# Performance work log

Hardware: AMD Instinct MI355X
Metric: run time of the kernel (lower is better)

Reference implementation:

```python
import jax, jax.numpy as jnp
import numpy as np

B = 1024          # batch
N = 2048          # number of gene groups
G = 32            # uniform group size (sum of gene_groups = N*G = 65536)
H1 = 2048         # hidden1_size
H2 = 512          # hidden2_size
EPS = 1e-5        # BatchNorm eps
SLOPE = 0.05      # LeakyReLU negative slope


def lrelu(v):
    return jnp.where(v >= 0, v, SLOPE * v)


def setup_inputs() -> dict:
    key = jax.random.key(0)
    ks = jax.random.split(key, 12)
    x = jax.random.normal(ks[0], (B, N * G), dtype=jnp.float32)
    # per-group Linear(G, 1) weights, stacked: [N, G] weights + [N] biases
    Wg = jax.random.normal(ks[1], (N, G), dtype=jnp.float32) / np.sqrt(G)
    bg = jax.random.normal(ks[2], (N,), dtype=jnp.float32) * 0.01
    att_w = jax.random.normal(ks[3], (N,), dtype=jnp.float32)
    W1 = jax.random.normal(ks[4], (N, H1), dtype=jnp.float32) / np.sqrt(N)
    b1 = jnp.zeros((H1,), dtype=jnp.float32)
    W2 = jax.random.normal(ks[5], (H1, H2), dtype=jnp.float32) / np.sqrt(H1)
    b2 = jnp.zeros((H2,), dtype=jnp.float32)
    Wo = jax.random.normal(ks[6], (H2, 1), dtype=jnp.float32) / np.sqrt(H2)
    bo = jnp.zeros((1,), dtype=jnp.float32)
    gamma1 = jnp.ones((H1,), dtype=jnp.float32)
    beta1 = jnp.zeros((H1,), dtype=jnp.float32)
    gamma2 = jnp.ones((H2,), dtype=jnp.float32)
    beta2 = jnp.zeros((H2,), dtype=jnp.float32)
    return dict(x=x, Wg=Wg, bg=bg, att_w=att_w, W1=W1, b1=b1,
                gamma1=gamma1, beta1=beta1, W2=W2, b2=b2,
                gamma2=gamma2, beta2=beta2, Wo=Wo, bo=bo)


def batchnorm(h, gamma, beta):
    # training-mode BatchNorm1d: batch statistics, biased variance
    mu = jnp.mean(h, axis=0)
    var = jnp.mean(jnp.square(h - mu), axis=0)
    return (h - mu) * jax.lax.rsqrt(var + EPS) * gamma + beta


def reference(x, Wg, bg, att_w, W1, b1, gamma1, beta1, W2, b2, gamma2, beta2, Wo, bo):
    # fused per-group linear + LeakyReLU: x viewed as [B, N, G]
    xg = x.reshape(B, N, G)
    g = lrelu(jnp.einsum('bng,ng->bn', xg, Wg) + bg)       # [B, N]
    att = jax.nn.softmax(att_w)                             # [N]
    a = g * att                                             # [B, N]
    h1 = lrelu(batchnorm(a @ W1 + b1, gamma1, beta1))       # [B, H1]
    h2 = lrelu(batchnorm(h1 @ W2 + b2, gamma2, beta2))      # [B, H2]
    return h2 @ Wo + bo                                     # [B, 1]
```

## Files before the change

kernel.cpp:

```cpp
#include <hip/hip_runtime.h>
#include <hip/hip_bf16.h>

#define B_DIM   1024
#define N_DIM   2048
#define G_DIM   32
#define H1_DIM  2048
#define H2_DIM  512
#define BN_EPS  1e-5f
#define SLOPE   0.05f

typedef short v8s __attribute__((ext_vector_type(8)));
typedef float v4f __attribute__((ext_vector_type(4)));

__device__ __forceinline__ float lrelu_f(float v) { return v >= 0.f ? v : SLOPE * v; }
__device__ __forceinline__ float bf2f(unsigned short u) {
    union { unsigned int i; float f; } c; c.i = ((unsigned int)u) << 16; return c.f;
}
__device__ __forceinline__ unsigned short f2bf(float f) {
    __hip_bfloat16 h = __float2bfloat16(f);
    return *(unsigned short*)&h;
}

#define GLOAD_LDS16(gp, lp)                                                              \
    __builtin_amdgcn_global_load_lds(                                                    \
        (const __attribute__((address_space(1))) unsigned int*)(gp),                     \
        (__attribute__((address_space(3))) unsigned int*)(lp), 16, 0, 0)

__global__ __launch_bounds__(256) void fused_transpose(
        const float* __restrict__ W1, const float* __restrict__ W2,
        const float* __restrict__ aw,
        __hip_bfloat16* __restrict__ W1T, __hip_bfloat16* __restrict__ W2T) {
    __shared__ float tile[64][65];
    __shared__ float red[8];
    __shared__ float scl[64];
    int t = threadIdx.x;
    int bid = blockIdx.x;
    const float* W;
    __hip_bfloat16* Wt;
    int Kd, Jd, j0, k0;
    bool doScale;
    if (bid < 1024) {
        W = W1; Wt = W1T; Kd = N_DIM; Jd = H1_DIM;
        j0 = (bid & 31) * 64; k0 = (bid >> 5) * 64; doScale = true;
        float mx = -1e30f;
#pragma unroll
        for (int i = 0; i < 8; ++i) mx = fmaxf(mx, aw[t + i * 256]);
#pragma unroll
        for (int off = 32; off; off >>= 1) mx = fmaxf(mx, __shfl_xor(mx, off, 64));
        if ((t & 63) == 0) red[t >> 6] = mx;
        __syncthreads();
        float M = fmaxf(fmaxf(red[0], red[1]), fmaxf(red[2], red[3]));
        float sm = 0.f;
#pragma unroll
        for (int i = 0; i < 8; ++i) sm += expf(aw[t + i * 256] - M);
#pragma unroll
        for (int off = 32; off; off >>= 1) sm += __shfl_xor(sm, off, 64);
        if ((t & 63) == 0) red[4 + (t >> 6)] = sm;
        __syncthreads();
        float invS = 1.f / (red[4] + red[5] + red[6] + red[7]);
        if (t < 64) scl[t] = expf(aw[k0 + t] - M) * invS;
        __syncthreads();
    } else {
        int b2 = bid - 1024;
        W = W2; Wt = W2T; Kd = H1_DIM; Jd = H2_DIM;
        j0 = (b2 & 7) * 64; k0 = (b2 >> 3) * 64; doScale = false;
    }
#pragma unroll
    for (int p = 0; p < 16; ++p) {
        int r = (t >> 6) + p * 4;
        float v = W[(size_t)(k0 + r) * Jd + j0 + (t & 63)];
        if (doScale) v *= scl[r];
        tile[r][t & 63] = v;
    }
    __syncthreads();
#pragma unroll
    for (int p = 0; p < 8; ++p) {
        int jr = (t >> 5) + p * 8;
        int kc = (t & 31) * 2;
        ushort2 pk;
        pk.x = f2bf(tile[kc][jr]);
        pk.y = f2bf(tile[kc + 1][jr]);
        *(ushort2*)(Wt + (size_t)(j0 + jr) * Kd + k0 + kc) = pk;
    }
}

__global__ __launch_bounds__(256) void group_linear(const float* __restrict__ x,
                                                    const float* __restrict__ Wg,
                                                    const float* __restrict__ bg,
                                                    __hip_bfloat16* __restrict__ g) {
    int t = threadIdx.x;
    int seg = blockIdx.y;
    int brow = blockIdx.x;
    int gl = t >> 1, half = t & 1;
    int n = seg * 128 + gl;
    float4 wv[4];
    const float4* wsrc = (const float4*)(Wg + (size_t)n * 32 + half * 16);
#pragma unroll
    for (int q = 0; q < 4; ++q) wv[q] = wsrc[q];
    float bgv = bg[n];
#pragma unroll
    for (int bb = 0; bb < 8; ++bb) {
        int b = brow * 8 + bb;
        const float4* xr = (const float4*)(x + (size_t)b * (N_DIM * G_DIM) + (size_t)n * 32 + half * 16);
        float s = 0.f;
#pragma unroll
        for (int q = 0; q < 4; ++q) {
            float4 v = xr[q];
            s += v.x * wv[q].x + v.y * wv[q].y + v.z * wv[q].z + v.w * wv[q].w;
        }
        s += __shfl_xor(s, 1, 64);
        if (half == 0)
            g[(size_t)b * N_DIM + n] = __float2bfloat16(lrelu_f(s + bgv));
    }
}

template<int BN_T, int TT, typename OutT>
__global__ __launch_bounds__(TT) void gemm_stats(
        const __hip_bfloat16* __restrict__ A, const __hip_bfloat16* __restrict__ Bt,
        OutT* __restrict__ C, float* __restrict__ ps, float* __restrict__ pq,
        int N, int K) {
    constexpr int WC = BN_T / 32;
    constexpr int WR = TT / 64 / WC;
    __shared__ __hip_bfloat16 A_s[2][64 * 128];
    __shared__ __hip_bfloat16 B_s[2][BN_T * 128];
    __shared__ float rs[WR][BN_T], rq[WR][BN_T];

    int nwg = gridDim.x * gridDim.y;
    int bid = blockIdx.y * gridDim.x + blockIdx.x;
    int cpx = nwg >> 3;
    int wg  = (bid & 7) * cpx + (bid >> 3);
    int bx  = wg % gridDim.x, by = wg / gridDim.x;

    int tid = threadIdx.x, lane = tid & 63, wave = tid >> 6;
    int wr = wave / WC, wc = wave % WC;
    int rbase = bx * 64, cbase = by * BN_T;
    int l15 = lane & 15, kq = lane >> 4;

    v4f acc[2][2] = {};

    auto stage = [&](int buf, int kt) {
        int k0 = kt << 7;
#pragma unroll
        for (int i = 0; i < 1024 / TT; ++i) {
            int s = tid + i * TT;
            int row = s >> 4, cg = (s & 15) ^ (row & 15);
            GLOAD_LDS16(A + (size_t)(rbase + row) * K + k0 + cg * 8, (char*)A_s[buf] + s * 16);
        }
#pragma unroll
        for (int i = 0; i < BN_T * 16 / TT; ++i) {
            int s = tid + i * TT;
            int row = s >> 4, cg = (s & 15) ^ (row & 15);
            GLOAD_LDS16(Bt + (size_t)(cbase + row) * K + k0 + cg * 8, (char*)B_s[buf] + s * 16);
        }
    };

    const int nkt = K >> 7;
    stage(0, 0);
    __syncthreads();
    int cur = 0;
    for (int kt = 0; kt < nkt; ++kt) {
        if (kt + 1 < nkt) stage(cur ^ 1, kt + 1);
#pragma unroll
        for (int kc = 0; kc < 4; ++kc) {
            v8s af[2], bfv[2];
#pragma unroll
            for (int m = 0; m < 2; ++m) {
                int row = wr * 32 + m * 16 + l15;
                int off = row * 256 + (((kc * 4 + kq) ^ (row & 15)) << 4);
                af[m] = *(const v8s*)((const char*)A_s[cur] + off);
            }
#pragma unroll
            for (int n = 0; n < 2; ++n) {
                int row = wc * 32 + n * 16 + l15;
                int off = row * 256 + (((kc * 4 + kq) ^ (row & 15)) << 4);
                bfv[n] = *(const v8s*)((const char*)B_s[cur] + off);
            }
            __builtin_amdgcn_s_setprio(1);
#pragma unroll
            for (int m = 0; m < 2; ++m)
#pragma unroll
                for (int n = 0; n < 2; ++n)
                    acc[m][n] = __builtin_amdgcn_mfma_f32_16x16x32_bf16(af[m], bfv[n],
                                                                        acc[m][n], 0, 0, 0);
            __builtin_amdgcn_s_setprio(0);
        }
        __syncthreads();
        cur ^= 1;
    }

    int crow = kq * 4;
#pragma unroll
    for (int m = 0; m < 2; ++m)
#pragma unroll
        for (int n = 0; n < 2; ++n) {
            int r = rbase + wr * 32 + m * 16 + crow;
            int c = cbase + wc * 32 + n * 16 + l15;
#pragma unroll
            for (int i = 0; i < 4; ++i) {
                float v = acc[m][n][i];
                if constexpr (sizeof(OutT) == 2)
                    ((__hip_bfloat16*)C)[(size_t)(r + i) * N + c] = __float2bfloat16(v);
                else
                    ((float*)C)[(size_t)(r + i) * N + c] = v;
            }
        }

    float cs[2], cq[2];
#pragma unroll
    for (int n = 0; n < 2; ++n) {
        cs[n] = 0.f; cq[n] = 0.f;
#pragma unroll
        for (int m = 0; m < 2; ++m)
#pragma unroll
            for (int i = 0; i < 4; ++i) {
                float v = acc[m][n][i];
                cs[n] += v; cq[n] += v * v;
            }
#pragma unroll
        for (int off = 16; off <= 32; off <<= 1) {
            cs[n] += __shfl_xor(cs[n], off, 64);
            cq[n] += __shfl_xor(cq[n], off, 64);
        }
    }
    if (lane < 16) {
#pragma unroll
        for (int n = 0; n < 2; ++n) {
            rs[wr][wc * 32 + n * 16 + lane] = cs[n];
            rq[wr][wc * 32 + n * 16 + lane] = cq[n];
        }
    }
    __syncthreads();
    if (tid < BN_T) {
        float s = 0.f, q = 0.f;
#pragma unroll
        for (int w = 0; w < WR; ++w) { s += rs[w][tid]; q += rq[w][tid]; }
        ps[(size_t)bx * N + cbase + tid] = s;
        pq[(size_t)bx * N + cbase + tid] = q;
    }
}

__global__ __launch_bounds__(256) void bn_apply_fused(
        const __hip_bfloat16* __restrict__ hpre,
        const float* __restrict__ ps, const float* __restrict__ pq,
        const float* __restrict__ gamma, const float* __restrict__ beta,
        __hip_bfloat16* __restrict__ o) {
    __shared__ float scl[H1_DIM], shf[H1_DIM];
    int t = threadIdx.x;
#pragma unroll
    for (int p = 0; p < 8; ++p) {
        int c = t + p * 256;
        float s = 0.f, q = 0.f;
#pragma unroll
        for (int i = 0; i < 16; ++i) {
            s += ps[i * H1_DIM + c];
            q += pq[i * H1_DIM + c];
        }
        float mu = s * (1.f / B_DIM);
        float var = fmaxf(q * (1.f / B_DIM) - mu * mu, 0.f);
        float rsv = rsqrtf(var + BN_EPS);
        float sc = rsv * gamma[c];
        scl[c] = sc;
        shf[c] = beta[c] - mu * sc;
    }
    __syncthreads();
    int j = t * 8;
    float4 sc0 = *(const float4*)&scl[j];
    float4 sc1 = *(const float4*)&scl[j + 4];
    float4 sh0 = *(const float4*)&shf[j];
    float4 sh1 = *(const float4*)&shf[j + 4];
#pragma unroll
    for (int rr = 0; rr < 8; ++rr) {
        size_t base = (size_t)(blockIdx.x * 8 + rr) * H1_DIM + j;
        v8s v = *(const v8s*)(hpre + base);
        v8s pk;
        pk[0] = (short)f2bf(lrelu_f(bf2f((unsigned short)v[0]) * sc0.x + sh0.x));
        pk[1] = (short)f2bf(lrelu_f(bf2f((unsigned short)v[1]) * sc0.y + sh0.y));
        pk[2] = (short)f2bf(lrelu_f(bf2f((unsigned short)v[2]) * sc0.z + sh0.z));
        pk[3] = (short)f2bf(lrelu_f(bf2f((unsigned short)v[3]) * sc0.w + sh0.w));
        pk[4] = (short)f2bf(lrelu_f(bf2f((unsigned short)v[4]) * sc1.x + sh1.x));
        pk[5] = (short)f2bf(lrelu_f(bf2f((unsigned short)v[5]) * sc1.y + sh1.y));
        pk[6] = (short)f2bf(lrelu_f(bf2f((unsigned short)v[6]) * sc1.z + sh1.z));
        pk[7] = (short)f2bf(lrelu_f(bf2f((unsigned short)v[7]) * sc1.w + sh1.w));
        *(v8s*)(o + base) = pk;
    }
}

__global__ __launch_bounds__(256) void bn_dot_fused(
        const float* __restrict__ h2,
        const float* __restrict__ ps, const float* __restrict__ pq,
        const float* __restrict__ gamma, const float* __restrict__ beta,
        const float* __restrict__ Wo, const float* __restrict__ bo,
        float* __restrict__ out) {
    __shared__ float scl[H2_DIM], shf[H2_DIM];
    __shared__ float red[4][4];
    int t = threadIdx.x;
#pragma unroll
    for (int p = 0; p < 2; ++p) {
        int c = t + p * 256;
        float s = 0.f, q = 0.f;
#pragma unroll
        for (int i = 0; i < 16; ++i) {
            s += ps[i * H2_DIM + c];
            q += pq[i * H2_DIM + c];
        }
        float mu = s * (1.f / B_DIM);
        float var = fmaxf(q * (1.f / B_DIM) - mu * mu, 0.f);
        float rsv = rsqrtf(var + BN_EPS);
        float sc = rsv * gamma[c];
        scl[c] = sc;
        shf[c] = beta[c] - mu * sc;
    }
    __syncthreads();
    float accv[4];
#pragma unroll
    for (int r = 0; r < 4; ++r) {
        int b = blockIdx.x * 4 + r;
        float s = 0.f;
#pragma unroll
        for (int p = 0; p < 2; ++p) {
            int jj = t + p * 256;
            float v = lrelu_f(h2[(size_t)b * H2_DIM + jj] * scl[jj] + shf[jj]);
            s += v * Wo[jj];
        }
#pragma unroll
        for (int off = 32; off; off >>= 1) s += __shfl_down(s, off, 64);
        accv[r] = s;
    }
    if ((t & 63) == 0) {
#pragma unroll
        for (int r = 0; r < 4; ++r) red[t >> 6][r] = accv[r];
    }
    __syncthreads();
    if (t < 4)
        out[blockIdx.x * 4 + t] = red[0][t] + red[1][t] + red[2][t] + red[3][t] + bo[0];
}

extern "C" void kernel_launch(void* const* d_in, const int* in_sizes, int n_in,
                              void* d_out, int out_size, void* d_ws, size_t ws_size,
                              hipStream_t stream) {
    const float* x     = (const float*)d_in[0];
    const float* Wg    = (const float*)d_in[1];
    const float* bg    = (const float*)d_in[2];
    const float* att_w = (const float*)d_in[3];
    const float* W1    = (const float*)d_in[4];
    const float* gamma1 = (const float*)d_in[6];
    const float* beta1  = (const float*)d_in[7];
    const float* W2    = (const float*)d_in[8];
    const float* gamma2 = (const float*)d_in[10];
    const float* beta2  = (const float*)d_in[11];
    const float* Wo    = (const float*)d_in[12];
    const float* bo    = (const float*)d_in[13];
    float* out = (float*)d_out;

    char* ws = (char*)d_ws;
    size_t off = 0;
    auto alloc = [&](size_t bytes) {
        void* p = ws + off;
        off = (off + bytes + 255) & ~(size_t)255;
        return p;
    };
    __hip_bfloat16* W1T    = (__hip_bfloat16*)alloc((size_t)H1_DIM * N_DIM * 2);
    __hip_bfloat16* W2T    = (__hip_bfloat16*)alloc((size_t)H2_DIM * H1_DIM * 2);
    __hip_bfloat16* g      = (__hip_bfloat16*)alloc((size_t)B_DIM * N_DIM * 2);
    __hip_bfloat16* h1pre  = (__hip_bfloat16*)alloc((size_t)B_DIM * H1_DIM * 2);
    __hip_bfloat16* h1     = (__hip_bfloat16*)alloc((size_t)B_DIM * H1_DIM * 2);
    float*          h2raw  = (float*)alloc((size_t)B_DIM * H2_DIM * 4);
    float*          ps     = (float*)alloc(16 * H1_DIM * 4);
    float*          pq     = (float*)alloc(16 * H1_DIM * 4);
    (void)ws_size; (void)in_sizes; (void)n_in; (void)out_size;

    fused_transpose<<<dim3(1024 + 256), 256, 0, stream>>>(W1, W2, att_w, W1T, W2T);
    group_linear<<<dim3(B_DIM / 8, N_DIM / 128), 256, 0, stream>>>(x, Wg, bg, g);
    gemm_stats<64, 256, __hip_bfloat16><<<dim3(B_DIM / 64, H1_DIM / 64), 256, 0, stream>>>(
        g, W1T, h1pre, ps, pq, H1_DIM, N_DIM);
    bn_apply_fused<<<dim3(B_DIM / 8), 256, 0, stream>>>(h1pre, ps, pq, gamma1, beta1, h1);
    gemm_stats<32, 128, float><<<dim3(B_DIM / 64, H2_DIM / 32), 128, 0, stream>>>(
        h1, W2T, h2raw, ps, pq, H2_DIM, H1_DIM);
    bn_dot_fused<<<dim3(B_DIM / 4), 256, 0, stream>>>(h2raw, ps, pq, gamma2, beta2, Wo, bo, out);
}
```

Before: 113.5 us.

## Merge group-linear into prep kernel and add dedicated 64x128 GEMM1 kernel

Folds the group-linear reduction and the weight transpose/softmax-scaling into one launch, so the two independent prep stages run concurrently and one kernel launch goes away. Replaces the templated first GEMM with a dedicated kernel using 512 threads, 64x128 output tiles and a K-step of 64, double-buffered with direct global-to-LDS loads and an XOR swizzle. The GEMM grid drops to 256 workgroups, which roughly matches the CU count but leaves no spare waves to hide latency. The merged prep kernel must size its LDS for the transpose path even on the group-linear blocks, which may lower occupancy for those blocks.

Measured after the change: 114.7 us. No clear change (+1.1%).

```diff
diff --git a/kernel.cpp b/kernel.cpp
--- a/kernel.cpp
+++ b/kernel.cpp
@@ -26,7 +26,9 @@
         (const __attribute__((address_space(1))) unsigned int*)(gp),                     \
         (__attribute__((address_space(3))) unsigned int*)(lp), 16, 0, 0)
 
-__global__ __launch_bounds__(256) void fused_transpose(
+__global__ __launch_bounds__(256) void prep_kernel(
+        const float* __restrict__ x, const float* __restrict__ Wg,
+        const float* __restrict__ bg, __hip_bfloat16* __restrict__ g,
         const float* __restrict__ W1, const float* __restrict__ W2,
         const float* __restrict__ aw,
         __hip_bfloat16* __restrict__ W1T, __hip_bfloat16* __restrict__ W2T) {
@@ -35,13 +37,43 @@
     __shared__ float scl[64];
     int t = threadIdx.x;
     int bid = blockIdx.x;
+
+    if (bid < 2048) {
+        int brow = bid >> 4;
+        int seg = bid & 15;
+        int gl = t >> 1, half = t & 1;
+        int n = seg * 128 + gl;
+        float4 wv[4];
+        const float4* wsrc = (const float4*)(Wg + (size_t)n * 32 + half * 16);
+#pragma unroll
+        for (int q = 0; q < 4; ++q) wv[q] = wsrc[q];
+        float bgv = bg[n];
+#pragma unroll
+        for (int bb = 0; bb < 8; ++bb) {
+            int b = brow * 8 + bb;
+            const float4* xr = (const float4*)(x + (size_t)b * (N_DIM * G_DIM) +
+                                               (size_t)n * 32 + half * 16);
+            float s = 0.f;
+#pragma unroll
+            for (int q = 0; q < 4; ++q) {
+                float4 v = xr[q];
+                s += v.x * wv[q].x + v.y * wv[q].y + v.z * wv[q].z + v.w * wv[q].w;
+            }
+            s += __shfl_xor(s, 1, 64);
+            if (half == 0)
+                g[(size_t)b * N_DIM + n] = __float2bfloat16(lrelu_f(s + bgv));
+        }
+        return;
+    }
+
     const float* W;
     __hip_bfloat16* Wt;
     int Kd, Jd, j0, k0;
     bool doScale;
-    if (bid < 1024) {
+    int tb = bid - 2048;
+    if (tb < 1024) {
         W = W1; Wt = W1T; Kd = N_DIM; Jd = H1_DIM;
-        j0 = (bid & 31) * 64; k0 = (bid >> 5) * 64; doScale = true;
+        j0 = (tb & 31) * 64; k0 = (tb >> 5) * 64; doScale = true;
         float mx = -1e30f;
 #pragma unroll
         for (int i = 0; i < 8; ++i) mx = fmaxf(mx, aw[t + i * 256]);
@@ -61,7 +93,7 @@
         if (t < 64) scl[t] = expf(aw[k0 + t] - M) * invS;
         __syncthreads();
     } else {
-        int b2 = bid - 1024;
+        int b2 = tb - 1024;
         W = W2; Wt = W2T; Kd = H1_DIM; Jd = H2_DIM;
         j0 = (b2 & 7) * 64; k0 = (b2 >> 3) * 64; doScale = false;
     }
@@ -84,33 +116,114 @@
     }
 }
 
-__global__ __launch_bounds__(256) void group_linear(const float* __restrict__ x,
-                                                    const float* __restrict__ Wg,
-                                                    const float* __restrict__ bg,
-                                                    __hip_bfloat16* __restrict__ g) {
-    int t = threadIdx.x;
-    int seg = blockIdx.y;
-    int brow = blockIdx.x;
-    int gl = t >> 1, half = t & 1;
-    int n = seg * 128 + gl;
-    float4 wv[4];
-    const float4* wsrc = (const float4*)(Wg + (size_t)n * 32 + half * 16);
-#pragma unroll
-    for (int q = 0; q < 4; ++q) wv[q] = wsrc[q];
-    float bgv = bg[n];
-#pragma unroll
-    for (int bb = 0; bb < 8; ++bb) {
-        int b = brow * 8 + bb;
-        const float4* xr = (const float4*)(x + (size_t)b * (N_DIM * G_DIM) + (size_t)n * 32 + half * 16);
-        float s = 0.f;
-#pragma unroll
-        for (int q = 0; q < 4; ++q) {
-            float4 v = xr[q];
-            s += v.x * wv[q].x + v.y * wv[q].y + v.z * wv[q].z + v.w * wv[q].w;
-        }
-        s += __shfl_xor(s, 1, 64);
-        if (half == 0)
-            g[(size_t)b * N_DIM + n] = __float2bfloat16(lrelu_f(s + bgv));
+__global__ __launch_bounds__(512) void gemm1_stats(
+        const __hip_bfloat16* __restrict__ A, const __hip_bfloat16* __restrict__ Bt,
+        __hip_bfloat16* __restrict__ C, float* __restrict__ ps, float* __restrict__ pq,
+        int N, int K) {
+    __shared__ __hip_bfloat16 A_s[2][64 * 64];
+    __shared__ __hip_bfloat16 B_s[2][128 * 64];
+    __shared__ float rs[2][128], rq[2][128];
+
+    int bid = blockIdx.y * 16 + blockIdx.x;
+    int wg  = (bid & 7) * 32 + (bid >> 3);
+    int bx  = wg & 15, by = wg >> 4;
+
+    int tid = threadIdx.x, lane = tid & 63, wave = tid >> 6;
+    int wr = wave >> 2, wc = wave & 3;
+    int rbase = bx * 64, cbase = by * 128;
+    int l15 = lane & 15, kq = lane >> 4;
+
+    v4f acc[2][2] = {};
+
+    auto stage = [&](int buf, int kt) {
+        int k0 = kt << 6;
+        {
+            int s = tid;
+            int row = s >> 3, cg = (s & 7) ^ (row & 7);
+            GLOAD_LDS16(A + (size_t)(rbase + row) * K + k0 + cg * 8, (char*)A_s[buf] + s * 16);
+        }
+#pragma unroll
+        for (int i = 0; i < 2; ++i) {
+            int s = tid + i * 512;
+            int row = s >> 3, cg = (s & 7) ^ (row & 7);
+            GLOAD_LDS16(Bt + (size_t)(cbase + row) * K + k0 + cg * 8, (char*)B_s[buf] + s * 16);
+        }
+    };
+
+    const int nkt = K >> 6;
+    stage(0, 0);
+    __syncthreads();
+    int cur = 0;
+    for (int kt = 0; kt < nkt; ++kt) {
+        if (kt + 1 < nkt) stage(cur ^ 1, kt + 1);
+#pragma unroll
+        for (int kc = 0; kc < 2; ++kc) {
+            v8s af[2], bfv[2];
+#pragma unroll
+            for (int m = 0; m < 2; ++m) {
+                int row = wr * 32 + m * 16 + l15;
+                int off = row * 128 + ((((kc << 2) + kq) ^ (row & 7)) << 4);
+                af[m] = *(const v8s*)((const char*)A_s[cur] + off);
+            }
+#pragma unroll
+            for (int n = 0; n < 2; ++n) {
+                int row = wc * 32 + n * 16 + l15;
+                int off = row * 128 + ((((kc << 2) + kq) ^ (row & 7)) << 4);
+                bfv[n] = *(const v8s*)((const char*)B_s[cur] + off);
+            }
+            __builtin_amdgcn_s_setprio(1);
+#pragma unroll
+            for (int m = 0; m < 2; ++m)
+#pragma unroll
+                for (int n = 0; n < 2; ++n)
+                    acc[m][n] = __builtin_amdgcn_mfma_f32_16x16x32_bf16(af[m], bfv[n],
+                                                                        acc[m][n], 0, 0, 0);
+            __builtin_amdgcn_s_setprio(0);
+        }
+        __syncthreads();
+        cur ^= 1;
+    }
+
+    int crow = kq * 4;
+#pragma unroll
+    for (int m = 0; m < 2; ++m)
+#pragma unroll
+        for (int n = 0; n < 2; ++n) {
+            int r = rbase + wr * 32 + m * 16 + crow;
+            int c = cbase + wc * 32 + n * 16 + l15;
+#pragma unroll
+            for (int i = 0; i < 4; ++i)
+                C[(size_t)(r + i) * N + c] = __float2bfloat16(acc[m][n][i]);
+        }
+
+    float cs[2], cq[2];
+#pragma unroll
+    for (int n = 0; n < 2; ++n) {
+        cs[n] = 0.f; cq[n] = 0.f;
+#pragma unroll
+        for (int m = 0; m < 2; ++m)
+#pragma unroll
+            for (int i = 0; i < 4; ++i) {
+                float v = acc[m][n][i];
+                cs[n] += v; cq[n] += v * v;
+            }
+#pragma unroll
+        for (int off = 16; off <= 32; off <<= 1) {
+            cs[n] += __shfl_xor(cs[n], off, 64);
+            cq[n] += __shfl_xor(cq[n], off, 64);
+        }
+    }
+    if (lane < 16) {
+#pragma unroll
+        for (int n = 0; n < 2; ++n) {
+            rs[wr][wc * 32 + n * 16 + lane] = cs[n];
+            rq[wr][wc * 32 + n * 16 + lane] = cq[n];
+        }
+    }
+    __syncthreads();
+    if (tid < 128) {
+        ps[(size_t)bx * N + cbase + tid] = rs[0][tid] + rs[1][tid];
+        pq[(size_t)bx * N + cbase + tid] = rq[0][tid] + rq[1][tid];
     }
 }
 
@@ -369,10 +482,9 @@
     float*          pq     = (float*)alloc(16 * H1_DIM * 4);
     (void)ws_size; (void)in_sizes; (void)n_in; (void)out_size;
 
-    fused_transpose<<<dim3(1024 + 256), 256, 0, stream>>>(W1, W2, att_w, W1T, W2T);
-    group_linear<<<dim3(B_DIM / 8, N_DIM / 128), 256, 0, stream>>>(x, Wg, bg, g);
-    gemm_stats<64, 256, __hip_bfloat16><<<dim3(B_DIM / 64, H1_DIM / 64), 256, 0, stream>>>(
-        g, W1T, h1pre, ps, pq, H1_DIM, N_DIM);
+    prep_kernel<<<dim3(2048 + 1024 + 256), 256, 0, stream>>>(x, Wg, bg, g,
+                                                             W1, W2, att_w, W1T, W2T);
+    gemm1_stats<<<dim3(16, 16), 512, 0, stream>>>(g, W1T, h1pre, ps, pq, H1_DIM, N_DIM);
     bn_apply_fused<<<dim3(B_DIM / 8), 256, 0, stream>>>(h1pre, ps, pq, gamma1, beta1, h1);
     gemm_stats<32, 128, float><<<dim3(B_DIM / 64, H2_DIM / 32), 128, 0, stream>>>(
         h1, W2T, h2raw, ps, pq, H2_DIM, H1_DIM);
```
